# Kernel optimization log

Hardware: AMD Instinct MI355X
Metric: run time of the kernel (lower is better)

The kernel has to match this reference:

```python
import jax, jax.numpy as jnp
import numpy as np

B, T, C, H = 8, 512, 1024, 16
N = C // H
DW, DA, DG = 64, 64, 128  # LoRA dims for decay / icl-rate / gate at C=1024

def _ln(x, w, b, eps=1e-5):
    mu = x.mean(-1, keepdims=True)
    var = ((x - mu) ** 2).mean(-1, keepdims=True)
    return (x - mu) * jax.lax.rsqrt(var + eps) * w + b

def _gn_heads(x, w, b, eps=64e-5):
    # GroupNorm(H groups) over channel dim of (B,T,C)
    xh = x.reshape(x.shape[0], x.shape[1], H, N)
    mu = xh.mean(-1, keepdims=True)
    var = ((xh - mu) ** 2).mean(-1, keepdims=True)
    xh = (xh - mu) * jax.lax.rsqrt(var + eps)
    return xh.reshape(x.shape) * w + b

def _shift(x):
    # RWKV time_shift: ZeroPad2d((0,0,1,-1))
    return jnp.concatenate([jnp.zeros_like(x[:, :1]), x[:, :-1]], axis=1)

def _wkv7(r, w_log, k, v, a, b):
    # all (B,T,H,N); state S (B,H,N,N): S = S*diag(exp(-exp(w))) + (S@a)b^T + v k^T; out = S@r
    decay = jnp.exp(-jnp.exp(w_log))
    def step(state, inp):
        r_t, d_t, k_t, v_t, a_t, b_t = inp
        sa = jnp.einsum('bhij,bhj->bhi', state, a_t)
        state = (state * d_t[:, :, None, :]
                 + sa[..., None] * b_t[:, :, None, :]
                 + v_t[..., None] * k_t[:, :, None, :])
        return state, jnp.einsum('bhij,bhj->bhi', state, r_t)
    xs = tuple(jnp.moveaxis(t, 1, 0) for t in (r, decay, k, v, a, b))
    s0 = jnp.zeros((r.shape[0], H, N, N), r.dtype)
    _, out = jax.lax.scan(step, s0, xs)
    return jnp.moveaxis(out, 0, 1)

def reference(x, v_first, ln_pre_w, ln_pre_b, ln_attn_w, ln_attn_b, ln_ffn_w, ln_ffn_b,
              x_r, x_w, x_k, x_v, x_a, x_g, w0, w1, w2, a0, a1, a2, g1, g2,
              k_k, k_a, r_k, W_r, W_k, W_v, W_o, gn_w, gn_b,
              ffn_x_k, W_ffn1, W_ffn2):
    Bx, Tx = x.shape[0], x.shape[1]
    x = _ln(x, ln_pre_w, ln_pre_b)            # pre_norm (layer_idx==0)
    # --- time mixing (RWKV7Attention) ---
    xn = _ln(x, ln_attn_w, ln_attn_b)
    dx = _shift(xn) - xn
    xr = xn + dx * x_r; xw = xn + dx * x_w; xk = xn + dx * x_k
    xv = xn + dx * x_v; xa = xn + dx * x_a; xg = xn + dx * x_g
    r = xr @ W_r
    w_log = -jax.nn.softplus(-(w0 + jnp.tanh(xw @ w1) @ w2)) - 0.5
    k = xk @ W_k
    v = xv @ W_v
    v_first = v                               # layer 0 stores v
    a = jax.nn.sigmoid(a0 + (xa @ a1) @ a2)   # in-context learning rate
    g = jax.nn.sigmoid(xg @ g1) @ g2          # gate
    kk = (k * k_k).reshape(Bx, Tx, H, N)
    kk = kk / jnp.maximum(jnp.linalg.norm(kk, axis=-1, keepdims=True), 1e-12)
    k = k * (1.0 + (a - 1.0) * k_a)
    rh = r.reshape(Bx, Tx, H, N)
    kh = k.reshape(Bx, Tx, H, N)
    vh = v.reshape(Bx, Tx, H, N)
    ah = a.reshape(Bx, Tx, H, N)
    o = _wkv7(rh, w_log.reshape(Bx, Tx, H, N), kh, vh, -kk, kk * ah)
    o = _gn_heads(o.reshape(Bx, Tx, C), gn_w, gn_b)
    o = o + ((rh * kh * r_k).sum(-1, keepdims=True) * vh).reshape(Bx, Tx, C)
    x = x + (o * g) @ W_o                     # residual (dropout p=0)
    # --- channel mixing (RWKV7FeedForward) ---
    xf = _ln(x, ln_ffn_w, ln_ffn_b)
    kf = xf + (_shift(xf) - xf) * ffn_x_k
    x = x + jnp.square(jax.nn.relu(kf @ W_ffn1)) @ W_ffn2
    return x, v_first

def setup_inputs() -> dict:
    key = jax.random.key(0)
    ks = iter(jax.random.split(key, 40))
    def nrm(shape, s=0.02):
        return jax.random.normal(next(ks), shape, jnp.float32) * s
    f32 = jnp.float32
    d = {
        'x': jax.random.normal(next(ks), (B, T, C), f32),
        'v_first': jnp.zeros((B, T, C), f32),
        'ln_pre_w': jnp.ones((C,), f32), 'ln_pre_b': jnp.zeros((C,), f32),
        'ln_attn_w': jnp.ones((C,), f32), 'ln_attn_b': jnp.zeros((C,), f32),
        'ln_ffn_w': jnp.ones((C,), f32), 'ln_ffn_b': jnp.zeros((C,), f32),
        'x_r': nrm((C,), 0.1), 'x_w': nrm((C,), 0.1), 'x_k': nrm((C,), 0.1),
        'x_v': nrm((C,), 0.1), 'x_a': nrm((C,), 0.1), 'x_g': nrm((C,), 0.1),
        'w0': nrm((C,), 0.5), 'w1': nrm((C, DW)), 'w2': nrm((DW, C)),
        'a0': nrm((C,), 0.1), 'a1': nrm((C, DA)), 'a2': nrm((DA, C)),
        'g1': nrm((C, DG)), 'g2': nrm((DG, C)),
        'k_k': 0.85 * jnp.ones((C,), f32) + nrm((C,), 0.05),
        'k_a': jnp.ones((C,), f32),
        'r_k': nrm((H, N), 0.1),
        'W_r': nrm((C, C)), 'W_k': nrm((C, C)), 'W_v': nrm((C, C)), 'W_o': nrm((C, C)),
        'gn_w': jnp.ones((C,), f32), 'gn_b': jnp.zeros((C,), f32),
        'ffn_x_k': nrm((C,), 0.1),
        'W_ffn1': nrm((C, 4 * C)), 'W_ffn2': nrm((4 * C, C)),
    }
    return d
```

## Files before the change

kernel.cpp:

```cpp
#include <hip/hip_runtime.h>

#define Bb 8
#define Tt 512
#define Cc 1024
#define Hh 16
#define Nh 64
#define Mm 4096
#define BTC 4194304
#define DEV __device__ __forceinline__

typedef __attribute__((ext_vector_type(8))) short short8;
typedef __attribute__((ext_vector_type(4))) float f32x4;

DEV unsigned short f2bf(float f) {
  unsigned int u = __builtin_bit_cast(unsigned int, f);
  u += 0x7fffu + ((u >> 16) & 1u);
  return (unsigned short)(u >> 16);
}

template <int CTRL>
DEV float dppadd(float x) {
  int xi = __builtin_bit_cast(int, x);
  int yi = __builtin_amdgcn_update_dpp(0, xi, CTRL, 0xF, 0xF, true);
  return x + __builtin_bit_cast(float, yi);
}

struct TDesc { const float* in; unsigned short* out; int K, N, bstart, nbx; };
struct TPack { TDesc d[12]; };

__global__ __launch_bounds__(256) void kt_transpose_multi(TPack p) {
  __shared__ float tile[32][33];
  const int bid = blockIdx.x;
  int i = 0;
  #pragma unroll
  for (int j = 1; j < 12; ++j) if (bid >= p.d[j].bstart) i = j;
  const float* in = p.d[i].in;
  unsigned short* out = p.d[i].out;
  const int K = p.d[i].K, N = p.d[i].N;
  const int local = bid - p.d[i].bstart;
  const int byq = local / p.d[i].nbx;
  const int bx = (local - byq * p.d[i].nbx) * 32;
  const int by = byq * 32;
  int tx = threadIdx.x, ty = threadIdx.y;
  #pragma unroll
  for (int q = ty; q < 32; q += 8) {
    int kk = by + q, nn = bx + tx;
    tile[q][tx] = (kk < K && nn < N) ? in[(size_t)kk * N + nn] : 0.f;
  }
  __syncthreads();
  #pragma unroll
  for (int q = ty; q < 32; q += 8) {
    int nn = bx + q, kk = by + tx;
    if (nn < N && kk < K) out[(size_t)nn * K + kk] = f2bf(tile[tx][q]);
  }
}

DEV void row_stats(float v0, float v1, float v2, float v3, float* red,
                   float& mu, float& rs, float eps) {
  float s = v0 + v1 + v2 + v3;
  float q = v0 * v0 + v1 * v1 + v2 * v2 + v3 * v3;
  #pragma unroll
  for (int o = 32; o; o >>= 1) { s += __shfl_down(s, o); q += __shfl_down(q, o); }
  int w = threadIdx.x >> 6;
  __syncthreads();
  if ((threadIdx.x & 63) == 0) { red[w] = s; red[4 + w] = q; }
  __syncthreads();
  s = red[0] + red[1] + red[2] + red[3];
  q = red[4] + red[5] + red[6] + red[7];
  mu = s * (1.f / 1024.f);
  float var = q * (1.f / 1024.f) - mu * mu;
  rs = rsqrtf(var + eps);
}

__global__ __launch_bounds__(256) void k1_mix(
    const float* __restrict__ x,
    const float* __restrict__ lnpw, const float* __restrict__ lnpb,
    const float* __restrict__ lnaw, const float* __restrict__ lnab,
    const float* __restrict__ cr, const float* __restrict__ cw,
    const float* __restrict__ ck, const float* __restrict__ cv,
    const float* __restrict__ ca, const float* __restrict__ cg,
    float* __restrict__ xln,
    unsigned short* __restrict__ mR, unsigned short* __restrict__ mW,
    unsigned short* __restrict__ mK, unsigned short* __restrict__ mV,
    unsigned short* __restrict__ mA, unsigned short* __restrict__ mG) {
  __shared__ float red[8];
  const int row = blockIdx.x;
  const int t = row & (Tt - 1);
  const int tid = threadIdx.x;
  const int c = tid * 4;
  const size_t base = (size_t)row * Cc + c;
  float a0 = x[base], a1 = x[base + 1], a2 = x[base + 2], a3 = x[base + 3];
  float mu, rs;
  row_stats(a0, a1, a2, a3, red, mu, rs, 1e-5f);
  float pw0 = lnpw[c], pw1 = lnpw[c + 1], pw2 = lnpw[c + 2], pw3 = lnpw[c + 3];
  float pb0 = lnpb[c], pb1 = lnpb[c + 1], pb2 = lnpb[c + 2], pb3 = lnpb[c + 3];
  float l0 = (a0 - mu) * rs * pw0 + pb0, l1 = (a1 - mu) * rs * pw1 + pb1;
  float l2 = (a2 - mu) * rs * pw2 + pb2, l3 = (a3 - mu) * rs * pw3 + pb3;
  float4 st; st.x = l0; st.y = l1; st.z = l2; st.w = l3;
  *(float4*)(xln + base) = st;
  row_stats(l0, l1, l2, l3, red, mu, rs, 1e-5f);
  float aw0 = lnaw[c], aw1 = lnaw[c + 1], aw2 = lnaw[c + 2], aw3 = lnaw[c + 3];
  float ab0 = lnab[c], ab1 = lnab[c + 1], ab2 = lnab[c + 2], ab3 = lnab[c + 3];
  float n0 = (l0 - mu) * rs * aw0 + ab0, n1 = (l1 - mu) * rs * aw1 + ab1;
  float n2 = (l2 - mu) * rs * aw2 + ab2, n3 = (l3 - mu) * rs * aw3 + ab3;
  float p0 = 0.f, p1 = 0.f, p2 = 0.f, p3 = 0.f;
  if (t > 0) {
    const size_t pb_ = base - Cc;
    float q0 = x[pb_], q1 = x[pb_ + 1], q2 = x[pb_ + 2], q3 = x[pb_ + 3];
    row_stats(q0, q1, q2, q3, red, mu, rs, 1e-5f);
    float e0 = (q0 - mu) * rs * pw0 + pb0, e1 = (q1 - mu) * rs * pw1 + pb1;
    float e2 = (q2 - mu) * rs * pw2 + pb2, e3 = (q3 - mu) * rs * pw3 + pb3;
    row_stats(e0, e1, e2, e3, red, mu, rs, 1e-5f);
    p0 = (e0 - mu) * rs * aw0 + ab0; p1 = (e1 - mu) * rs * aw1 + ab1;
    p2 = (e2 - mu) * rs * aw2 + ab2; p3 = (e3 - mu) * rs * aw3 + ab3;
  }
  float d0 = p0 - n0, d1 = p1 - n1, d2 = p2 - n2, d3 = p3 - n3;
  #define EMIT(cf, dst) { \
    float f0 = cf[c], f1 = cf[c + 1], f2 = cf[c + 2], f3 = cf[c + 3]; \
    ushort4 u; u.x = f2bf(n0 + d0 * f0); u.y = f2bf(n1 + d1 * f1); \
    u.z = f2bf(n2 + d2 * f2); u.w = f2bf(n3 + d3 * f3); \
    *(ushort4*)(dst + base) = u; }
  EMIT(cr, mR) EMIT(cw, mW) EMIT(ck, mK) EMIT(cv, mV) EMIT(ca, mA) EMIT(cg, mG)
  #undef EMIT
}

DEV void gll16(const unsigned short* g, unsigned short* l) {
  __builtin_amdgcn_global_load_lds(
      (const __attribute__((address_space(1))) void*)g,
      (__attribute__((address_space(3))) void*)l, 16, 0, 0);
}

template <int MODE>
DEV void gemm_epi(float z, size_t oi, int col,
                  float* outF, unsigned short* outB,
                  const float* bias, const float* res) {
  if constexpr (MODE == 0) outF[oi] = z;
  else if constexpr (MODE == 1) outB[oi] = f2bf(z);
  else if constexpr (MODE == 2) outB[oi] = f2bf(tanhf(z));
  else if constexpr (MODE == 3) outB[oi] = f2bf(1.f / (1.f + expf(-z)));
  else if constexpr (MODE == 4) { float m = fmaxf(z, 0.f); outB[oi] = f2bf(m * m); }
  else if constexpr (MODE == 5) { z += bias[col]; outF[oi] = 1.f / (1.f + expf(-z)); }
  else if constexpr (MODE == 6) {
    z += bias[col];
    float sg = 1.f / (1.f + expf(-z));
    outF[oi] = expf(-0.6065306597126334f * sg);
  } else { outF[oi] = z + res[oi]; }
}

DEV void gemm_epi_rt(int mode, float z, size_t oi, int col,
                     float* outF, unsigned short* outB, const float* bias) {
  if (mode == 0) outF[oi] = z;
  else if (mode == 1) outB[oi] = f2bf(z);
  else if (mode == 2) outB[oi] = f2bf(tanhf(z));
  else if (mode == 3) outB[oi] = f2bf(1.f / (1.f + expf(-z)));
  else if (mode == 5) { z += bias[col]; outF[oi] = 1.f / (1.f + expf(-z)); }
  else { z += bias[col]; float sg = 1.f / (1.f + expf(-z));
         outF[oi] = expf(-0.6065306597126334f * sg); }
}

DEV void gemm_body_rt(const unsigned short* A, const unsigned short* Bt,
                      int Nn, int K,
                      float* outF, unsigned short* outB, const float* bias,
                      unsigned short* lsA, unsigned short* lsB,
                      int m0, int n0, int mode) {
  const int tid = threadIdx.x;
  const int lane = tid & 63;
  const int wave = tid >> 6;
  const int wy = wave >> 1, wx = wave & 1;
  const int sl4 = lane >> 2;
  const int sc = (lane & 3) << 3;
  f32x4 acc[4][2];
  #pragma unroll
  for (int i = 0; i < 4; ++i)
    #pragma unroll
    for (int j = 0; j < 2; ++j) { f32x4 z = {0.f, 0.f, 0.f, 0.f}; acc[i][j] = z; }
  const int fr = lane & 15;
  const int fk = (lane >> 4) << 3;
  for (int k0 = 0; k0 < K; k0 += 32) {
    #pragma unroll
    for (int j = 0; j < 2; ++j) {
      const int rb = (wave + j * 4) * 16;
      gll16(A + (size_t)(m0 + rb + sl4) * K + k0 + sc, lsA + rb * 32);
    }
    {
      const int rb = wave * 16;
      int br = n0 + rb + sl4;
      br = br < Nn ? br : Nn - 1;
      gll16(Bt + (size_t)br * K + k0 + sc, lsB + rb * 32);
    }
    __syncthreads();
    short8 af[4], bf[2];
    #pragma unroll
    for (int mt = 0; mt < 4; ++mt)
      af[mt] = *(const short8*)(lsA + (wy * 64 + mt * 16 + fr) * 32 + fk);
    #pragma unroll
    for (int nt = 0; nt < 2; ++nt)
      bf[nt] = *(const short8*)(lsB + (wx * 32 + nt * 16 + fr) * 32 + fk);
    #pragma unroll
    for (int mt = 0; mt < 4; ++mt)
      #pragma unroll
      for (int nt = 0; nt < 2; ++nt)
        acc[mt][nt] = __builtin_amdgcn_mfma_f32_16x16x32_bf16(af[mt], bf[nt], acc[mt][nt], 0, 0, 0);
    __syncthreads();
  }
  const int rbase = (lane >> 4) << 2;
  const int cbase = lane & 15;
  #pragma unroll
  for (int mt = 0; mt < 4; ++mt)
    #pragma unroll
    for (int nt = 0; nt < 2; ++nt)
      #pragma unroll
      for (int rr = 0; rr < 4; ++rr) {
        int row = m0 + wy * 64 + mt * 16 + rbase + rr;
        int col = n0 + wx * 32 + nt * 16 + cbase;
        if (col < Nn)
          gemm_epi_rt(mode, acc[mt][nt][rr], (size_t)row * Nn + col, col, outF, outB, bias);
      }
}

__global__ __launch_bounds__(256) void kg_lora1(
    const unsigned short* __restrict__ mW, const unsigned short* __restrict__ mA,
    const unsigned short* __restrict__ mG,
    const unsigned short* __restrict__ w1T, const unsigned short* __restrict__ a1T,
    const unsigned short* __restrict__ g1T,
    unsigned short* __restrict__ tmpw, unsigned short* __restrict__ tmpa,
    unsigned short* __restrict__ tmpg) {
  __shared__ unsigned short lsA[128 * 32];
  __shared__ unsigned short lsB[64 * 32];
  const int z = blockIdx.z;
  const unsigned short* A  = z == 0 ? mW : z == 1 ? mA : mG;
  const unsigned short* Bt = z == 0 ? w1T : z == 1 ? a1T : g1T;
  unsigned short* outB     = z == 0 ? tmpw : z == 1 ? tmpa : tmpg;
  const int Nn = z < 2 ? 64 : 128;
  const int n0 = z < 2 ? 0 : (z - 2) * 64;
  const int mode = z == 0 ? 2 : z == 1 ? 1 : 3;
  gemm_body_rt(A, Bt, Nn, 1024, nullptr, outB, nullptr, lsA, lsB,
               blockIdx.y * 128, n0, mode);
}

__global__ __launch_bounds__(256) void kg_lora2(
    const unsigned short* __restrict__ tmpw, const unsigned short* __restrict__ tmpa,
    const unsigned short* __restrict__ tmpg,
    const unsigned short* __restrict__ w2T, const unsigned short* __restrict__ a2T,
    const unsigned short* __restrict__ g2T,
    float* __restrict__ decay, float* __restrict__ aicl, float* __restrict__ gout,
    const float* __restrict__ w0v, const float* __restrict__ a0v) {
  __shared__ unsigned short lsA[128 * 32];
  __shared__ unsigned short lsB[64 * 32];
  const int z = blockIdx.z;
  const unsigned short* A  = z == 0 ? tmpw : z == 1 ? tmpa : tmpg;
  const unsigned short* Bt = z == 0 ? w2T : z == 1 ? a2T : g2T;
  float* outF              = z == 0 ? decay : z == 1 ? aicl : gout;
  const float* bias        = z == 0 ? w0v : z == 1 ? a0v : nullptr;
  const int K = z < 2 ? 64 : 128;
  const int mode = z == 0 ? 6 : z == 1 ? 5 : 0;
  gemm_body_rt(A, Bt, 1024, K, outF, nullptr, bias, lsA, lsB,
               blockIdx.y * 128, blockIdx.x * 64, mode);
}

template <int MODE>
DEV void gemm2_body(const unsigned short* A, const unsigned short* Bt,
                    int Nn, int K,
                    float* outF, unsigned short* outB,
                    const float* bias, const float* res,
                    unsigned short* lsA, unsigned short* lsB,
                    int m0, int n0) {
  const int tid = threadIdx.x;
  const int lane = tid & 63;
  const int wave = tid >> 6;
  const int wy = wave >> 1, wx = wave & 1;
  const int sl4 = lane >> 2;
  const int sc = (lane & 3) << 3;
  f32x4 acc[4][4];
  #pragma unroll
  for (int i = 0; i < 4; ++i)
    #pragma unroll
    for (int j = 0; j < 4; ++j) { f32x4 z = {0.f, 0.f, 0.f, 0.f}; acc[i][j] = z; }
  const int fr = lane & 15;
  const int fk = (lane >> 4) << 3;
  for (int k0 = 0; k0 < K; k0 += 32) {
    #pragma unroll
    for (int j = 0; j < 2; ++j) {
      const int rb = (wave + j * 4) * 16;
      gll16(A + (size_t)(m0 + rb + sl4) * K + k0 + sc, lsA + rb * 32);
      int br = n0 + rb + sl4;
      br = br < Nn ? br : Nn - 1;
      gll16(Bt + (size_t)br * K + k0 + sc, lsB + rb * 32);
    }
    __syncthreads();
    short8 af[4], bf[4];
    #pragma unroll
    for (int mt = 0; mt < 4; ++mt)
      af[mt] = *(const short8*)(lsA + (wy * 64 + mt * 16 + fr) * 32 + fk);
    #pragma unroll
    for (int nt = 0; nt < 4; ++nt)
      bf[nt] = *(const short8*)(lsB + (wx * 64 + nt * 16 + fr) * 32 + fk);
    #pragma unroll
    for (int mt = 0; mt < 4; ++mt)
      #pragma unroll
      for (int nt = 0; nt < 4; ++nt)
        acc[mt][nt] = __builtin_amdgcn_mfma_f32_16x16x32_bf16(af[mt], bf[nt], acc[mt][nt], 0, 0, 0);
    __syncthreads();
  }
  const int rbase = (lane >> 4) << 2;
  const int cbase = lane & 15;
  #pragma unroll
  for (int mt = 0; mt < 4; ++mt)
    #pragma unroll
    for (int nt = 0; nt < 4; ++nt)
      #pragma unroll
      for (int rr = 0; rr < 4; ++rr) {
        int row = m0 + wy * 64 + mt * 16 + rbase + rr;
        int col = n0 + wx * 64 + nt * 16 + cbase;
        if (col < Nn)
          gemm_epi<MODE>(acc[mt][nt][rr], (size_t)row * Nn + col, col, outF, outB, bias, res);
      }
}

template <int MODE>
__global__ __launch_bounds__(256) void kg_gemm2(
    const unsigned short* __restrict__ A, const unsigned short* __restrict__ Bt,
    int M, int Nn, int K,
    float* __restrict__ outF, unsigned short* __restrict__ outB,
    const float* __restrict__ bias, const float* __restrict__ res) {
  __shared__ unsigned short lsA[128 * 32];
  __shared__ unsigned short lsB[128 * 32];
  gemm2_body<MODE>(A, Bt, Nn, K, outF, outB, bias, res, lsA, lsB,
                   blockIdx.y * 128, blockIdx.x * 128);
}

__global__ __launch_bounds__(256) void kg_gemm2_qkv(
    const unsigned short* __restrict__ A0, const unsigned short* __restrict__ A1,
    const unsigned short* __restrict__ A2,
    const unsigned short* __restrict__ B0, const unsigned short* __restrict__ B1,
    const unsigned short* __restrict__ B2,
    float* __restrict__ O0, float* __restrict__ O1, float* __restrict__ O2) {
  __shared__ unsigned short lsA[128 * 32];
  __shared__ unsigned short lsB[128 * 32];
  const int z = blockIdx.z;
  const unsigned short* A = z == 0 ? A0 : z == 1 ? A1 : A2;
  const unsigned short* Bt = z == 0 ? B0 : z == 1 ? B1 : B2;
  float* outF = z == 0 ? O0 : z == 1 ? O1 : O2;
  gemm2_body<0>(A, Bt, 1024, 1024, outF, nullptr, nullptr, nullptr, lsA, lsB,
                blockIdx.y * 128, blockIdx.x * 128);
}

__global__ __launch_bounds__(256) void k4_prep(
    float* __restrict__ k, const float* __restrict__ a,
    const float* __restrict__ kkc, const float* __restrict__ kac,
    float* __restrict__ aw, float* __restrict__ bw) {
  const int row = blockIdx.x, tid = threadIdx.x;
  const int c = tid * 4;
  const size_t base = (size_t)row * Cc + c;
  float k0 = k[base], k1 = k[base + 1], k2 = k[base + 2], k3 = k[base + 3];
  float a0 = a[base], a1 = a[base + 1], a2 = a[base + 2], a3 = a[base + 3];
  float h0 = k0 * kkc[c], h1 = k1 * kkc[c + 1], h2 = k2 * kkc[c + 2], h3 = k3 * kkc[c + 3];
  float ss = h0 * h0 + h1 * h1 + h2 * h2 + h3 * h3;
  #pragma unroll
  for (int m = 8; m; m >>= 1) ss += __shfl_xor(ss, m);
  float inv = 1.f / fmaxf(sqrtf(ss), 1e-12f);
  h0 *= inv; h1 *= inv; h2 *= inv; h3 *= inv;
  float4 v4;
  v4.x = -h0; v4.y = -h1; v4.z = -h2; v4.w = -h3;
  *(float4*)(aw + base) = v4;
  v4.x = h0 * a0; v4.y = h1 * a1; v4.z = h2 * a2; v4.w = h3 * a3;
  *(float4*)(bw + base) = v4;
  v4.x = k0 * (1.f + (a0 - 1.f) * kac[c]);
  v4.y = k1 * (1.f + (a1 - 1.f) * kac[c + 1]);
  v4.z = k2 * (1.f + (a2 - 1.f) * kac[c + 2]);
  v4.w = k3 * (1.f + (a3 - 1.f) * kac[c + 3]);
  *(float4*)(k + base) = v4;
}

#define CS 8
__global__ __launch_bounds__(512, 2) void k5_wkv7(
    const float* __restrict__ r, const float* __restrict__ dec,
    const float* __restrict__ k, const float* __restrict__ v,
    const float* __restrict__ aw, const float* __restrict__ bw,
    float* __restrict__ o) {
  const int blk = blockIdx.x;
  const int bh = blk & 127, half = blk >> 7;
  const int b = bh >> 4, h = bh & 15;
  const int tid = threadIdx.x;
  const int lane = tid & 63;
  const int w = tid >> 6;
  const int cg = lane & 15;
  const int rw = lane >> 4;
  const int row = half * 32 + w * 4 + rw;
  const int cb = cg << 2;

  __shared__ float buf[2][6 * CS * 64];

  float S[4];
  #pragma unroll
  for (int j = 0; j < 4; ++j) S[j] = 0.f;

  const size_t base = (size_t)b * Tt * Cc + (size_t)h * Nh;

  const float* sptr = w == 0 ? aw : w == 1 ? dec : w == 2 ? bw
                    : w == 3 ? k  : w == 4 ? r   : v;
  const int srow = lane >> 4;
  const int scol = (lane & 15) << 2;

  uint4 R0, R1;
  #define LOADC(cstart) if (w < 6) { \
    const size_t g0 = base + (size_t)((cstart) + srow) * Cc + scol; \
    R0 = *(const uint4*)(sptr + g0); \
    R1 = *(const uint4*)(sptr + g0 + 4 * Cc); }

  LOADC(0)

  #pragma unroll 1
  for (int c = 0; c < Tt / CS; ++c) {
    float* bp = buf[c & 1];
    if (w < 6) {
      *(uint4*)(bp + w * 512 + (lane << 2)) = R0;
      *(uint4*)(bp + w * 512 + 256 + (lane << 2)) = R1;
    }
    const int cn = (c + 1 < Tt / CS) ? (c + 1) : c;
    LOADC(cn * CS)
    __syncthreads();

    float4 Aq[2], Dq[2], Bq[2], Kq[2], Rq[2];
    float Vv[2];
    #define LOADOPS(slot, ss) { \
      const float* sp_ = bp + (ss) * 64; \
      Aq[slot] = *(const float4*)(sp_ + cb); \
      Dq[slot] = *(const float4*)(sp_ + 512 + cb); \
      Bq[slot] = *(const float4*)(sp_ + 1024 + cb); \
      Kq[slot] = *(const float4*)(sp_ + 1536 + cb); \
      Rq[slot] = *(const float4*)(sp_ + 2048 + cb); \
      Vv[slot] = sp_[2560 + row]; }

    LOADOPS(0, 0)
    #pragma unroll
    for (int s = 0; s < CS; ++s) {
      const int cu = s & 1, nx = cu ^ 1;
      if (s + 1 < CS) LOADOPS(nx, s + 1)

      float4 a4 = Aq[cu];
      float sa = fmaf(S[1], a4.y, S[0] * a4.x) + fmaf(S[3], a4.w, S[2] * a4.z);
      sa = dppadd<0xB1>(sa);
      sa = dppadd<0x4E>(sa);
      sa = dppadd<0x124>(sa);
      sa = dppadd<0x128>(sa);

      const float vv = Vv[cu];
      float4 d4 = Dq[cu], b4 = Bq[cu], k4 = Kq[cu], r4 = Rq[cu];
      S[0] = fmaf(S[0], d4.x, fmaf(vv, k4.x, sa * b4.x));
      float oo = S[0] * r4.x;
      S[1] = fmaf(S[1], d4.y, fmaf(vv, k4.y, sa * b4.y));
      oo = fmaf(S[1], r4.y, oo);
      S[2] = fmaf(S[2], d4.z, fmaf(vv, k4.z, sa * b4.z));
      oo = fmaf(S[2], r4.z, oo);
      S[3] = fmaf(S[3], d4.w, fmaf(vv, k4.w, sa * b4.w));
      oo = fmaf(S[3], r4.w, oo);

      oo = dppadd<0xB1>(oo);
      oo = dppadd<0x4E>(oo);
      oo = dppadd<0x124>(oo);
      oo = dppadd<0x128>(oo);
      if (cg == 0) o[base + (size_t)(c * CS + s) * Cc + row] = oo;
    }
    #undef LOADOPS
  }
  #undef LOADC
}

__global__ __launch_bounds__(256) void k6_out(
    const float* __restrict__ o, const float* __restrict__ r, const float* __restrict__ k,
    const float* __restrict__ v, const float* __restrict__ rk,
    const float* __restrict__ gnw, const float* __restrict__ gnb,
    const float* __restrict__ g, unsigned short* __restrict__ og) {
  const int row = blockIdx.x, tid = threadIdx.x;
  const int c = tid * 4;
  const size_t base = (size_t)row * Cc + c;
  float o0 = o[base], o1 = o[base + 1], o2 = o[base + 2], o3 = o[base + 3];
  float r0 = r[base], r1 = r[base + 1], r2 = r[base + 2], r3 = r[base + 3];
  float k0 = k[base], k1 = k[base + 1], k2 = k[base + 2], k3 = k[base + 3];
  float s = o0 + o1 + o2 + o3;
  float q = o0 * o0 + o1 * o1 + o2 * o2 + o3 * o3;
  float bs = r0 * k0 * rk[c] + r1 * k1 * rk[c + 1] + r2 * k2 * rk[c + 2] + r3 * k3 * rk[c + 3];
  #pragma unroll
  for (int m = 8; m; m >>= 1) {
    s += __shfl_xor(s, m); q += __shfl_xor(q, m); bs += __shfl_xor(bs, m);
  }
  float mu = s * (1.f / 64.f);
  float var = q * (1.f / 64.f) - mu * mu;
  float rs = rsqrtf(var + 64e-5f);
  float v0 = v[base], v1 = v[base + 1], v2 = v[base + 2], v3 = v[base + 3];
  float z0 = (o0 - mu) * rs * gnw[c] + gnb[c] + bs * v0;
  float z1 = (o1 - mu) * rs * gnw[c + 1] + gnb[c + 1] + bs * v1;
  float z2 = (o2 - mu) * rs * gnw[c + 2] + gnb[c + 2] + bs * v2;
  float z3 = (o3 - mu) * rs * gnw[c + 3] + gnb[c + 3] + bs * v3;
  ushort4 u;
  u.x = f2bf(z0 * g[base]); u.y = f2bf(z1 * g[base + 1]);
  u.z = f2bf(z2 * g[base + 2]); u.w = f2bf(z3 * g[base + 3]);
  *(ushort4*)(og + base) = u;
}

__global__ __launch_bounds__(256) void k8_ffnmix(
    const float* __restrict__ x2, const float* __restrict__ lnw, const float* __restrict__ lnb,
    const float* __restrict__ fxk, unsigned short* __restrict__ kf) {
  __shared__ float red[8];
  const int row = blockIdx.x;
  const int t = row & (Tt - 1);
  const int tid = threadIdx.x;
  const int c = tid * 4;
  const size_t base = (size_t)row * Cc + c;
  float a0 = x2[base], a1 = x2[base + 1], a2 = x2[base + 2], a3 = x2[base + 3];
  float mu, rs;
  row_stats(a0, a1, a2, a3, red, mu, rs, 1e-5f);
  float w0 = lnw[c], w1 = lnw[c + 1], w2 = lnw[c + 2], w3 = lnw[c + 3];
  float b0 = lnb[c], b1 = lnb[c + 1], b2 = lnb[c + 2], b3 = lnb[c + 3];
  float f0 = (a0 - mu) * rs * w0 + b0, f1 = (a1 - mu) * rs * w1 + b1;
  float f2 = (a2 - mu) * rs * w2 + b2, f3 = (a3 - mu) * rs * w3 + b3;
  float p0 = 0.f, p1 = 0.f, p2 = 0.f, p3 = 0.f;
  if (t > 0) {
    const size_t pb_ = base - Cc;
    float q0 = x2[pb_], q1 = x2[pb_ + 1], q2 = x2[pb_ + 2], q3 = x2[pb_ + 3];
    row_stats(q0, q1, q2, q3, red, mu, rs, 1e-5f);
    p0 = (q0 - mu) * rs * w0 + b0; p1 = (q1 - mu) * rs * w1 + b1;
    p2 = (q2 - mu) * rs * w2 + b2; p3 = (q3 - mu) * rs * w3 + b3;
  }
  ushort4 u;
  u.x = f2bf(f0 + (p0 - f0) * fxk[c]);
  u.y = f2bf(f1 + (p1 - f1) * fxk[c + 1]);
  u.z = f2bf(f2 + (p2 - f2) * fxk[c + 2]);
  u.w = f2bf(f3 + (p3 - f3) * fxk[c + 3]);
  *(ushort4*)(kf + base) = u;
}

extern "C" void kernel_launch(void* const* d_in, const int* in_sizes, int n_in,
                              void* d_out, int out_size, void* d_ws, size_t ws_size,
                              hipStream_t stream) {
  (void)in_sizes; (void)n_in; (void)out_size; (void)ws_size;
  const float* x    = (const float*)d_in[0];
  const float* lnpw = (const float*)d_in[2];
  const float* lnpb = (const float*)d_in[3];
  const float* lnaw = (const float*)d_in[4];
  const float* lnab = (const float*)d_in[5];
  const float* lnfw = (const float*)d_in[6];
  const float* lnfb = (const float*)d_in[7];
  const float* cxr  = (const float*)d_in[8];
  const float* cxw  = (const float*)d_in[9];
  const float* cxk  = (const float*)d_in[10];
  const float* cxv  = (const float*)d_in[11];
  const float* cxa  = (const float*)d_in[12];
  const float* cxg  = (const float*)d_in[13];
  const float* w0v  = (const float*)d_in[14];
  const float* w1m  = (const float*)d_in[15];
  const float* w2m  = (const float*)d_in[16];
  const float* a0v  = (const float*)d_in[17];
  const float* a1m  = (const float*)d_in[18];
  const float* a2m  = (const float*)d_in[19];
  const float* g1m  = (const float*)d_in[20];
  const float* g2m  = (const float*)d_in[21];
  const float* kkv  = (const float*)d_in[22];
  const float* kav  = (const float*)d_in[23];
  const float* rkv  = (const float*)d_in[24];
  const float* Wr   = (const float*)d_in[25];
  const float* Wk   = (const float*)d_in[26];
  const float* Wv   = (const float*)d_in[27];
  const float* Wo   = (const float*)d_in[28];
  const float* gnw  = (const float*)d_in[29];
  const float* gnb  = (const float*)d_in[30];
  const float* fxk  = (const float*)d_in[31];
  const float* Wf1  = (const float*)d_in[32];
  const float* Wf2  = (const float*)d_in[33];

  char* ws = (char*)d_ws;
  float* outx = (float*)d_out;
  float* vout = outx + BTC;

  size_t off = 0;
  unsigned short* WrT  = (unsigned short*)(ws + off); off += 2097152;
  unsigned short* WkT  = (unsigned short*)(ws + off); off += 2097152;
  unsigned short* WvT  = (unsigned short*)(ws + off); off += 2097152;
  unsigned short* WoT  = (unsigned short*)(ws + off); off += 2097152;
  unsigned short* Wf1T = (unsigned short*)(ws + off); off += 8388608;
  unsigned short* Wf2T = (unsigned short*)(ws + off); off += 8388608;
  unsigned short* w1T  = (unsigned short*)(ws + off); off += 131072;
  unsigned short* w2T  = (unsigned short*)(ws + off); off += 131072;
  unsigned short* a1T  = (unsigned short*)(ws + off); off += 131072;
  unsigned short* a2T  = (unsigned short*)(ws + off); off += 131072;
  unsigned short* g1T  = (unsigned short*)(ws + off); off += 262144;
  unsigned short* g2T  = (unsigned short*)(ws + off); off += 262144;
  float* xln = (float*)(ws + off); off += 16777216;
  unsigned short* mixR = (unsigned short*)(ws + off);
  unsigned short* mixW = (unsigned short*)(ws + off + 8388608);
  unsigned short* mixK = (unsigned short*)(ws + off + 16777216);
  unsigned short* mixV = (unsigned short*)(ws + off + 25165824);
  unsigned short* mixA = (unsigned short*)(ws + off + 33554432);
  unsigned short* mixG = (unsigned short*)(ws + off + 41943040);
  unsigned short* hbuf = (unsigned short*)(ws + off);
  off += 50331648;
  unsigned short* tmpw = (unsigned short*)(ws + off); off += 524288;
  unsigned short* tmpa = (unsigned short*)(ws + off); off += 524288;
  unsigned short* tmpg = (unsigned short*)(ws + off); off += 1048576;
  float* decay = (float*)(ws + off);
  unsigned short* og = (unsigned short*)(ws + off);
  off += 16777216;
  float* aicl = (float*)(ws + off);
  float* obuf = (float*)(ws + off);
  off += 16777216;
  float* gout = (float*)(ws + off); off += 16777216;
  float* rbuf = (float*)(ws + off);
  float* x2   = (float*)(ws + off);
  off += 16777216;
  float* kbuf = (float*)(ws + off); off += 16777216;
  float* awb  = (float*)(ws + off);
  unsigned short* kf = (unsigned short*)(ws + off);
  off += 16777216;
  float* bwb  = (float*)(ws + off); off += 16777216;

  dim3 tb(32, 8);
  TPack tp;
  tp.d[0]  = TDesc{Wr,  WrT,  1024, 1024, 0,     32};
  tp.d[1]  = TDesc{Wk,  WkT,  1024, 1024, 1024,  32};
  tp.d[2]  = TDesc{Wv,  WvT,  1024, 1024, 2048,  32};
  tp.d[3]  = TDesc{Wo,  WoT,  1024, 1024, 3072,  32};
  tp.d[4]  = TDesc{Wf1, Wf1T, 1024, 4096, 4096,  128};
  tp.d[5]  = TDesc{Wf2, Wf2T, 4096, 1024, 8192,  32};
  tp.d[6]  = TDesc{w1m, w1T,  1024, 64,   12288, 2};
  tp.d[7]  = TDesc{w2m, w2T,  64,   1024, 12352, 32};
  tp.d[8]  = TDesc{a1m, a1T,  1024, 64,   12416, 2};
  tp.d[9]  = TDesc{a2m, a2T,  64,   1024, 12480, 32};
  tp.d[10] = TDesc{g1m, g1T,  1024, 128,  12544, 4};
  tp.d[11] = TDesc{g2m, g2T,  128,  1024, 12672, 32};
  kt_transpose_multi<<<12800, tb, 0, stream>>>(tp);

  k1_mix<<<Mm, 256, 0, stream>>>(x, lnpw, lnpb, lnaw, lnab, cxr, cxw, cxk, cxv, cxa, cxg,
                                 xln, mixR, mixW, mixK, mixV, mixA, mixG);

  kg_lora1<<<dim3(1, 32, 4), 256, 0, stream>>>(mixW, mixA, mixG, w1T, a1T, g1T,
                                               tmpw, tmpa, tmpg);
  kg_lora2<<<dim3(16, 32, 3), 256, 0, stream>>>(tmpw, tmpa, tmpg, w2T, a2T, g2T,
                                                decay, aicl, gout, w0v, a0v);

  kg_gemm2_qkv<<<dim3(8, 32, 3), 256, 0, stream>>>(mixR, mixK, mixV, WrT, WkT, WvT,
                                                   rbuf, kbuf, vout);

  k4_prep<<<Mm, 256, 0, stream>>>(kbuf, aicl, kkv, kav, awb, bwb);
  k5_wkv7<<<256, 512, 0, stream>>>(rbuf, decay, kbuf, vout, awb, bwb, obuf);
  k6_out<<<Mm, 256, 0, stream>>>(obuf, rbuf, kbuf, vout, rkv, gnw, gnb, gout, og);
  kg_gemm2<7><<<dim3(8, 32), 256, 0, stream>>>(og, WoT, Mm, 1024, 1024, x2, nullptr, nullptr, xln);
  k8_ffnmix<<<Mm, 256, 0, stream>>>(x2, lnfw, lnfb, fxk, kf);
  kg_gemm2<4><<<dim3(32, 32), 256, 0, stream>>>(kf, Wf1T, Mm, 4096, 1024, nullptr, hbuf, nullptr, nullptr);
  kg_gemm2<7><<<dim3(8, 32), 256, 0, stream>>>(hbuf, Wf2T, Mm, 1024, 4096, outx, nullptr, nullptr, x2);
}
```

Baseline: 619.3 us.

## Fuse k-normalization prep into QKV GEMM epilogue and use 128x64 tiles for N=1024 GEMMs

```diff
diff --git a/kernel.cpp b/kernel.cpp
--- a/kernel.cpp
+++ b/kernel.cpp
@@ -158,6 +158,71 @@
          outF[oi] = expf(-0.6065306597126334f * sg); }
 }
 
+template <int MODE>
+__global__ __launch_bounds__(256) void kg_gemm64(
+    const unsigned short* __restrict__ A, const unsigned short* __restrict__ Bt,
+    int M, int Nn, int K,
+    float* __restrict__ outF, unsigned short* __restrict__ outB,
+    const float* __restrict__ bias, const float* __restrict__ res) {
+  __shared__ unsigned short lsA[128 * 32];
+  __shared__ unsigned short lsB[64 * 32];
+  const int tid = threadIdx.x;
+  const int lane = tid & 63;
+  const int wave = tid >> 6;
+  const int wy = wave >> 1, wx = wave & 1;
+  const int m0 = blockIdx.y * 128;
+  const int n0 = blockIdx.x * 64;
+  const int sl4 = lane >> 2;
+  const int sc = (lane & 3) << 3;
+  f32x4 acc[4][2];
+  #pragma unroll
+  for (int i = 0; i < 4; ++i)
+    #pragma unroll
+    for (int j = 0; j < 2; ++j) { f32x4 z = {0.f, 0.f, 0.f, 0.f}; acc[i][j] = z; }
+  const int fr = lane & 15;
+  const int fk = (lane >> 4) << 3;
+  for (int k0 = 0; k0 < K; k0 += 32) {
+    #pragma unroll
+    for (int j = 0; j < 2; ++j) {
+      const int rb = (wave + j * 4) * 16;
+      gll16(A + (size_t)(m0 + rb + sl4) * K + k0 + sc, lsA + rb * 32);
+    }
+    {
+      const int rb = wave * 16;
+      int br = n0 + rb + sl4;
+      br = br < Nn ? br : Nn - 1;
+      gll16(Bt + (size_t)br * K + k0 + sc, lsB + rb * 32);
+    }
+    __syncthreads();
+    short8 af[4], bf[2];
+    #pragma unroll
+    for (int mt = 0; mt < 4; ++mt)
+      af[mt] = *(const short8*)(lsA + (wy * 64 + mt * 16 + fr) * 32 + fk);
+    #pragma unroll
+    for (int nt = 0; nt < 2; ++nt)
+      bf[nt] = *(const short8*)(lsB + (wx * 32 + nt * 16 + fr) * 32 + fk);
+    #pragma unroll
+    for (int mt = 0; mt < 4; ++mt)
+      #pragma unroll
+      for (int nt = 0; nt < 2; ++nt)
+        acc[mt][nt] = __builtin_amdgcn_mfma_f32_16x16x32_bf16(af[mt], bf[nt], acc[mt][nt], 0, 0, 0);
+    __syncthreads();
+  }
+  const int rbase = (lane >> 4) << 2;
+  const int cbase = lane & 15;
+  #pragma unroll
+  for (int mt = 0; mt < 4; ++mt)
+    #pragma unroll
+    for (int nt = 0; nt < 2; ++nt)
+      #pragma unroll
+      for (int rr = 0; rr < 4; ++rr) {
+        int row = m0 + wy * 64 + mt * 16 + rbase + rr;
+        int col = n0 + wx * 32 + nt * 16 + cbase;
+        if (col < Nn)
+          gemm_epi<MODE>(acc[mt][nt][rr], (size_t)row * Nn + col, col, outF, outB, bias, res);
+      }
+}
+
 DEV void gemm_body_rt(const unsigned short* A, const unsigned short* Bt,
                       int Nn, int K,
                       float* outF, unsigned short* outB, const float* bias,
@@ -329,47 +394,107 @@
                    blockIdx.y * 128, blockIdx.x * 128);
 }
 
-__global__ __launch_bounds__(256) void kg_gemm2_qkv(
+__global__ __launch_bounds__(256) void kg_qkv_fused(
     const unsigned short* __restrict__ A0, const unsigned short* __restrict__ A1,
     const unsigned short* __restrict__ A2,
     const unsigned short* __restrict__ B0, const unsigned short* __restrict__ B1,
     const unsigned short* __restrict__ B2,
-    float* __restrict__ O0, float* __restrict__ O1, float* __restrict__ O2) {
+    float* __restrict__ rbuf, float* __restrict__ kbuf, float* __restrict__ vout,
+    const float* __restrict__ aicl,
+    const float* __restrict__ kkc, const float* __restrict__ kac,
+    float* __restrict__ awb, float* __restrict__ bwb) {
   __shared__ unsigned short lsA[128 * 32];
   __shared__ unsigned short lsB[128 * 32];
   const int z = blockIdx.z;
   const unsigned short* A = z == 0 ? A0 : z == 1 ? A1 : A2;
   const unsigned short* Bt = z == 0 ? B0 : z == 1 ? B1 : B2;
-  float* outF = z == 0 ? O0 : z == 1 ? O1 : O2;
-  gemm2_body<0>(A, Bt, 1024, 1024, outF, nullptr, nullptr, nullptr, lsA, lsB,
-                blockIdx.y * 128, blockIdx.x * 128);
-}
-
-__global__ __launch_bounds__(256) void k4_prep(
-    float* __restrict__ k, const float* __restrict__ a,
-    const float* __restrict__ kkc, const float* __restrict__ kac,
-    float* __restrict__ aw, float* __restrict__ bw) {
-  const int row = blockIdx.x, tid = threadIdx.x;
-  const int c = tid * 4;
-  const size_t base = (size_t)row * Cc + c;
-  float k0 = k[base], k1 = k[base + 1], k2 = k[base + 2], k3 = k[base + 3];
-  float a0 = a[base], a1 = a[base + 1], a2 = a[base + 2], a3 = a[base + 3];
-  float h0 = k0 * kkc[c], h1 = k1 * kkc[c + 1], h2 = k2 * kkc[c + 2], h3 = k3 * kkc[c + 3];
-  float ss = h0 * h0 + h1 * h1 + h2 * h2 + h3 * h3;
-  #pragma unroll
-  for (int m = 8; m; m >>= 1) ss += __shfl_xor(ss, m);
-  float inv = 1.f / fmaxf(sqrtf(ss), 1e-12f);
-  h0 *= inv; h1 *= inv; h2 *= inv; h3 *= inv;
-  float4 v4;
-  v4.x = -h0; v4.y = -h1; v4.z = -h2; v4.w = -h3;
-  *(float4*)(aw + base) = v4;
-  v4.x = h0 * a0; v4.y = h1 * a1; v4.z = h2 * a2; v4.w = h3 * a3;
-  *(float4*)(bw + base) = v4;
-  v4.x = k0 * (1.f + (a0 - 1.f) * kac[c]);
-  v4.y = k1 * (1.f + (a1 - 1.f) * kac[c + 1]);
-  v4.z = k2 * (1.f + (a2 - 1.f) * kac[c + 2]);
-  v4.w = k3 * (1.f + (a3 - 1.f) * kac[c + 3]);
-  *(float4*)(k + base) = v4;
+  const int tid = threadIdx.x;
+  const int lane = tid & 63;
+  const int wave = tid >> 6;
+  const int wy = wave >> 1, wx = wave & 1;
+  const int m0 = blockIdx.y * 128;
+  const int n0 = blockIdx.x * 128;
+  const int sl4 = lane >> 2;
+  const int sc = (lane & 3) << 3;
+  f32x4 acc[4][4];
+  #pragma unroll
+  for (int i = 0; i < 4; ++i)
+    #pragma unroll
+    for (int j = 0; j < 4; ++j) { f32x4 zz = {0.f, 0.f, 0.f, 0.f}; acc[i][j] = zz; }
+  const int fr = lane & 15;
+  const int fk = (lane >> 4) << 3;
+  for (int k0 = 0; k0 < 1024; k0 += 32) {
+    #pragma unroll
+    for (int j = 0; j < 2; ++j) {
+      const int rb = (wave + j * 4) * 16;
+      gll16(A + (size_t)(m0 + rb + sl4) * 1024 + k0 + sc, lsA + rb * 32);
+      gll16(Bt + (size_t)(n0 + rb + sl4) * 1024 + k0 + sc, lsB + rb * 32);
+    }
+    __syncthreads();
+    short8 af[4], bf[4];
+    #pragma unroll
+    for (int mt = 0; mt < 4; ++mt)
+      af[mt] = *(const short8*)(lsA + (wy * 64 + mt * 16 + fr) * 32 + fk);
+    #pragma unroll
+    for (int nt = 0; nt < 4; ++nt)
+      bf[nt] = *(const short8*)(lsB + (wx * 64 + nt * 16 + fr) * 32 + fk);
+    #pragma unroll
+    for (int mt = 0; mt < 4; ++mt)
+      #pragma unroll
+      for (int nt = 0; nt < 4; ++nt)
+        acc[mt][nt] = __builtin_amdgcn_mfma_f32_16x16x32_bf16(af[mt], bf[nt], acc[mt][nt], 0, 0, 0);
+    __syncthreads();
+  }
+  const int rbase = (lane >> 4) << 2;
+  const int cbase = lane & 15;
+  if (z != 1) {
+    float* outF = z == 0 ? rbuf : vout;
+    #pragma unroll
+    for (int mt = 0; mt < 4; ++mt)
+      #pragma unroll
+      for (int nt = 0; nt < 4; ++nt)
+        #pragma unroll
+        for (int rr = 0; rr < 4; ++rr) {
+          int row = m0 + wy * 64 + mt * 16 + rbase + rr;
+          int col = n0 + wx * 64 + nt * 16 + cbase;
+          outF[(size_t)row * Cc + col] = acc[mt][nt][rr];
+        }
+  } else {
+    float kkc4[4], kac4[4];
+    #pragma unroll
+    for (int nt = 0; nt < 4; ++nt) {
+      int col = n0 + wx * 64 + nt * 16 + cbase;
+      kkc4[nt] = kkc[col];
+      kac4[nt] = kac[col];
+    }
+    #pragma unroll
+    for (int mt = 0; mt < 4; ++mt)
+      #pragma unroll
+      for (int rr = 0; rr < 4; ++rr) {
+        int row = m0 + wy * 64 + mt * 16 + rbase + rr;
+        float h0 = acc[mt][0][rr] * kkc4[0];
+        float h1 = acc[mt][1][rr] * kkc4[1];
+        float h2 = acc[mt][2][rr] * kkc4[2];
+        float h3 = acc[mt][3][rr] * kkc4[3];
+        float ss = (h0 * h0 + h1 * h1) + (h2 * h2 + h3 * h3);
+        ss = dppadd<0xB1>(ss);
+        ss = dppadd<0x4E>(ss);
+        ss = dppadd<0x124>(ss);
+        ss = dppadd<0x128>(ss);
+        float inv = 1.f / fmaxf(sqrtf(ss), 1e-12f);
+        #pragma unroll
+        for (int nt = 0; nt < 4; ++nt) {
+          int col = n0 + wx * 64 + nt * 16 + cbase;
+          size_t oi = (size_t)row * Cc + col;
+          float kv = acc[mt][nt][rr];
+          float hn = kv * kkc4[nt] * inv;
+          float av = aicl[oi];
+          awb[oi] = -hn;
+          bwb[oi] = hn * av;
+          kbuf[oi] = kv * (1.f + (av - 1.f) * kac4[nt]);
+        }
+      }
+  }
 }
 
 #define CS 8
@@ -638,14 +763,14 @@
   kg_lora2<<<dim3(16, 32, 3), 256, 0, stream>>>(tmpw, tmpa, tmpg, w2T, a2T, g2T,
                                                 decay, aicl, gout, w0v, a0v);
 
-  kg_gemm2_qkv<<<dim3(8, 32, 3), 256, 0, stream>>>(mixR, mixK, mixV, WrT, WkT, WvT,
-                                                   rbuf, kbuf, vout);
-
-  k4_prep<<<Mm, 256, 0, stream>>>(kbuf, aicl, kkv, kav, awb, bwb);
+  kg_qkv_fused<<<dim3(8, 32, 3), 256, 0, stream>>>(mixR, mixK, mixV, WrT, WkT, WvT,
+                                                   rbuf, kbuf, vout,
+                                                   aicl, kkv, kav, awb, bwb);
+
   k5_wkv7<<<256, 512, 0, stream>>>(rbuf, decay, kbuf, vout, awb, bwb, obuf);
   k6_out<<<Mm, 256, 0, stream>>>(obuf, rbuf, kbuf, vout, rkv, gnw, gnb, gout, og);
-  kg_gemm2<7><<<dim3(8, 32), 256, 0, stream>>>(og, WoT, Mm, 1024, 1024, x2, nullptr, nullptr, xln);
+  kg_gemm64<7><<<dim3(16, 32), 256, 0, stream>>>(og, WoT, Mm, 1024, 1024, x2, nullptr, nullptr, xln);
   k8_ffnmix<<<Mm, 256, 0, stream>>>(x2, lnfw, lnfb, fxk, kf);
   kg_gemm2<4><<<dim3(32, 32), 256, 0, stream>>>(kf, Wf1T, Mm, 4096, 1024, nullptr, hbuf, nullptr, nullptr);
-  kg_gemm2<7><<<dim3(8, 32), 256, 0, stream>>>(hbuf, Wf2T, Mm, 1024, 4096, outx, nullptr, nullptr, x2);
-}
+  kg_gemm64<7><<<dim3(16, 32), 256, 0, stream>>>(hbuf, Wf2T, Mm, 1024, 4096, outx, nullptr, nullptr, x2);
+}
```

Result: faster. 585.8 us (-5.4%).
